# Performance work log

Hardware: AMD Instinct MI355X
Metric: run time of the kernel (lower is better)

The kernel has to match this reference:

```python
import jax, jax.numpy as jnp
import numpy as np

ALPHA = 0.2  # LeakyReLU negative slope
NEG_INF = -9e15

def setup_inputs() -> dict:
    key = jax.random.key(0)
    k1, k2, k3, k4 = jax.random.split(key, 4)
    N, IN_F, OUT_F = 12288, 256, 128
    h = jax.random.normal(k1, (N, IN_F), dtype=jnp.float32)
    adj = jax.random.randint(k2, (N, N), 0, 2, dtype=jnp.int32)
    # Xavier-uniform-like init with gain 1.414
    limW = 1.414 * np.sqrt(6.0 / (IN_F + OUT_F))
    W = jax.random.uniform(k3, (IN_F, OUT_F), dtype=jnp.float32, minval=-limW, maxval=limW)
    lima = 1.414 * np.sqrt(6.0 / (2 * OUT_F + 1))
    a = jax.random.uniform(k4, (2 * OUT_F, 1), dtype=jnp.float32, minval=-lima, maxval=lima)
    return {"h": h, "adj": adj, "W": W, "a": a}

def reference(h, adj, W, a):
    out_f = W.shape[1]
    Wh = h @ W                      # [N, out_f]
    Wh1 = Wh @ a[:out_f, :]         # [N, 1]
    Wh2 = Wh @ a[out_f:, :]         # [N, 1]
    e = Wh1 + Wh2.T                 # [N, N] broadcast-add scores
    e = jnp.where(e > 0, e, ALPHA * e)  # LeakyReLU
    scores = jnp.where(adj > 0, e, NEG_INF)
    attention = jax.nn.softmax(scores, axis=1)  # dropout is identity at inference
    h_prime = attention @ Wh        # [N, out_f]
    return jax.nn.elu(h_prime)      # concat=True -> ELU
```

## Files before the change

### kernel.cpp

```cpp
#include <hip/hip_runtime.h>

#define NN   12288
#define FIN  256
#define FOUT 128
#define ALPHA 0.2f

typedef __attribute__((ext_vector_type(8))) _Float16 half8v;
typedef __attribute__((ext_vector_type(4))) float float4v;
typedef __attribute__((ext_vector_type(4))) int   int4v;


__global__ __launch_bounds__(128) void k_wh(
    const float* __restrict__ h,
    const float* __restrict__ W,
    const float* __restrict__ a,
    _Float16* __restrict__ WhT2,
    float* __restrict__ Wh1, float* __restrict__ Wh2,
    float* __restrict__ mxArr)
{
    __shared__ float sP1[2][16], sP2[2][16];
    const int t = threadIdx.x;
    const int row0 = blockIdx.x * 16;

    float acc[16];
    #pragma unroll
    for (int r = 0; r < 16; ++r) acc[r] = 0.f;

    const float* hb = h + (size_t)row0 * FIN;
    for (int k = 0; k < FIN; k += 4) {
        const float w0 = W[(k + 0) * FOUT + t];
        const float w1 = W[(k + 1) * FOUT + t];
        const float w2 = W[(k + 2) * FOUT + t];
        const float w3 = W[(k + 3) * FOUT + t];
        #pragma unroll
        for (int r = 0; r < 16; ++r) {
            const float4v hv = *(const float4v*)(hb + r * FIN + k);
            float s = acc[r];
            s = fmaf(hv.x, w0, s);
            s = fmaf(hv.y, w1, s);
            s = fmaf(hv.z, w2, s);
            s = fmaf(hv.w, w3, s);
            acc[r] = s;
        }
    }

    half8v pk0, pk1;
    #pragma unroll
    for (int r = 0; r < 8; ++r)  pk0[r] = (_Float16)acc[r];
    #pragma unroll
    for (int r = 0; r < 8; ++r)  pk1[r] = (_Float16)acc[8 + r];
    _Float16* dst = WhT2 + (size_t)(row0 >> 5) * 4096 + t * 32 + (row0 & 16);
    *(half8v*)(dst)     = pk0;
    *(half8v*)(dst + 8) = pk1;

    const float a1t = a[t];
    const float a2t = a[FOUT + t];
    const int lane = t & 63, wv = t >> 6;
    #pragma unroll
    for (int r = 0; r < 16; ++r) {
        float v1 = acc[r] * a1t;
        float v2 = acc[r] * a2t;
        #pragma unroll
        for (int off = 1; off < 64; off <<= 1) {
            v1 += __shfl_xor(v1, off, 64);
            v2 += __shfl_xor(v2, off, 64);
        }
        if (lane == 0) { sP1[wv][r] = v1; sP2[wv][r] = v2; }
    }
    __syncthreads();
    if (t < 16) {
        const float v1 = sP1[0][t] + sP1[1][t];
        float v2 = sP2[0][t] + sP2[1][t];
        Wh1[row0 + t] = v1;
        Wh2[row0 + t] = v2;
        #pragma unroll
        for (int off = 1; off < 16; off <<= 1)
            v2 = fmaxf(v2, __shfl_xor(v2, off, 64));
        if (t == 0) mxArr[blockIdx.x] = v2;
    }
}

static __device__ __forceinline__ half8v build_p(
    const int4v a0, const int4v a1, const float* wvv,
    const float wh1, const float M, float& S)
{
    const int av[8] = {a0.x, a0.y, a0.z, a0.w, a1.x, a1.y, a1.z, a1.w};
    half8v af;
    #pragma unroll
    for (int jj = 0; jj < 8; ++jj) {
        float e = wh1 + wvv[jj];
        e = fmaxf(e, ALPHA * e);
        const float p = av[jj] ? __expf(e - M) : 0.f;
        af[jj] = (_Float16)p;
        S += p;
    }
    return af;
}

static __device__ __forceinline__ float block_gmax(
    const float* __restrict__ mxArr, int nmx, float* smax)
{
    const int tid = threadIdx.x;
    float mv = -1e30f;
    for (int idx = tid; idx < nmx; idx += 256) mv = fmaxf(mv, mxArr[idx]);
    #pragma unroll
    for (int off = 1; off < 64; off <<= 1) mv = fmaxf(mv, __shfl_xor(mv, off, 64));
    if ((tid & 63) == 0) smax[tid >> 6] = mv;
    __syncthreads();
    return fmaxf(fmaxf(smax[0], smax[1]), fmaxf(smax[2], smax[3]));
}

__global__ __launch_bounds__(256, 3) void k_attn(
    const int* __restrict__ adj,
    const _Float16* __restrict__ WhT2,
    const float* __restrict__ Wh1, const float* __restrict__ Wh2,
    const float* __restrict__ mxArr, int nmx,
    float* __restrict__ pC, float* __restrict__ pS)
{
    __shared__ float smax[4];
    const int tid  = threadIdx.x;
    const int w    = tid >> 6;
    const int lane = tid & 63;
    const int m    = lane & 15;
    const int q    = lane >> 4;
    const int rowbase = blockIdx.x * 64 + w * 16;
    const int J    = gridDim.y;
    const int jy   = blockIdx.y;
    const int jlen = NN / J;
    const int jbeg = jy * jlen;

    const float mxv = block_gmax(mxArr, nmx, smax);

    const float wh1 = Wh1[rowbase + m];
    const float tm  = wh1 + mxv;
    const float Mi  = fmaxf(tm, ALPHA * tm);
    const int* rowA = adj + (size_t)(rowbase + m) * NN;

    float4v c[8];
    #pragma unroll
    for (int t = 0; t < 8; ++t) c[t] = (float4v){0.f, 0.f, 0.f, 0.f};
    float S = 0.f;

    for (int j0 = jbeg; j0 < jbeg + jlen; j0 += 32) {
        const int jb = j0 + q * 8;
        const int4v a0 = __builtin_nontemporal_load((const int4v*)(rowA + jb));
        const int4v a1 = __builtin_nontemporal_load((const int4v*)(rowA + jb + 4));
        const float4v w0 = *(const float4v*)(Wh2 + jb);
        const float4v w1 = *(const float4v*)(Wh2 + jb + 4);
        const float wvv[8] = {w0.x, w0.y, w0.z, w0.w, w1.x, w1.y, w1.z, w1.w};

        const half8v af = build_p(a0, a1, wvv, wh1, Mi, S);

        const _Float16* tp = WhT2 + (size_t)(j0 >> 5) * 4096;
        #pragma unroll
        for (int t = 0; t < 8; ++t) {
            const half8v b = *(const half8v*)(tp + (t * 16 + m) * 32 + q * 8);
            c[t] = __builtin_amdgcn_mfma_f32_16x16x32_f16(af, b, c[t], 0, 0, 0);
        }
    }

    S += __shfl_xor(S, 16, 64);
    S += __shfl_xor(S, 32, 64);
    if (q == 0) pS[(size_t)jy * NN + rowbase + m] = S;

    #pragma unroll
    for (int t = 0; t < 8; ++t)
        #pragma unroll
        for (int reg = 0; reg < 4; ++reg) {
            const int row = rowbase + q * 4 + reg;
            pC[((size_t)jy * NN + row) * FOUT + t * 16 + m] = c[t][reg];
        }
}

__global__ __launch_bounds__(256) void k_reduce(
    const float* __restrict__ pC, const float* __restrict__ pS,
    float* __restrict__ out, int J)
{
    const int idx = blockIdx.x * 256 + threadIdx.x;
    const int row = idx >> 5;
    const int c4  = (idx & 31) * 4;
    float4v acc = (float4v){0.f, 0.f, 0.f, 0.f};
    float S = 0.f;
    for (int j = 0; j < J; ++j) {
        const float4v v = *(const float4v*)(pC + ((size_t)j * NN + row) * FOUT + c4);
        acc.x += v.x; acc.y += v.y; acc.z += v.z; acc.w += v.w;
        S += pS[(size_t)j * NN + row];
    }
    const float inv = 1.f / fmaxf(S, 1e-30f);
    float4v r;
    #pragma unroll
    for (int k = 0; k < 4; ++k) {
        const float v = acc[k] * inv;
        r[k] = (v > 0.f) ? v : (__expf(v) - 1.f);
    }
    *(float4v*)(out + (size_t)row * FOUT + c4) = r;
}

__global__ __launch_bounds__(256, 3) void k_attn_fb(
    const int* __restrict__ adj,
    const _Float16* __restrict__ WhT2,
    const float* __restrict__ Wh1, const float* __restrict__ Wh2,
    const float* __restrict__ mxArr, int nmx,
    float* __restrict__ out)
{
    __shared__ float smax[4];
    const int tid  = threadIdx.x;
    const int w    = tid >> 6;
    const int lane = tid & 63;
    const int m    = lane & 15;
    const int q    = lane >> 4;
    const int rowbase = blockIdx.x * 64 + w * 16;

    const float mxv = block_gmax(mxArr, nmx, smax);

    const float wh1 = Wh1[rowbase + m];
    const float tm  = wh1 + mxv;
    const float Mi  = fmaxf(tm, ALPHA * tm);
    const int* rowA = adj + (size_t)(rowbase + m) * NN;

    float4v c[8];
    #pragma unroll
    for (int t = 0; t < 8; ++t) c[t] = (float4v){0.f, 0.f, 0.f, 0.f};
    float S = 0.f;

    for (int j0 = 0; j0 < NN; j0 += 32) {
        const int jb = j0 + q * 8;
        const int4v a0 = __builtin_nontemporal_load((const int4v*)(rowA + jb));
        const int4v a1 = __builtin_nontemporal_load((const int4v*)(rowA + jb + 4));
        const float4v w0 = *(const float4v*)(Wh2 + jb);
        const float4v w1 = *(const float4v*)(Wh2 + jb + 4);
        const float wvv[8] = {w0.x, w0.y, w0.z, w0.w, w1.x, w1.y, w1.z, w1.w};
        const half8v af = build_p(a0, a1, wvv, wh1, Mi, S);
        const _Float16* tp = WhT2 + (size_t)(j0 >> 5) * 4096;
        #pragma unroll
        for (int t = 0; t < 8; ++t) {
            const half8v b = *(const half8v*)(tp + (t * 16 + m) * 32 + q * 8);
            c[t] = __builtin_amdgcn_mfma_f32_16x16x32_f16(af, b, c[t], 0, 0, 0);
        }
    }
    S += __shfl_xor(S, 16, 64);
    S += __shfl_xor(S, 32, 64);
    #pragma unroll
    for (int reg = 0; reg < 4; ++reg) {
        const int mloc = q * 4 + reg;
        const float Sr = __shfl(S, mloc, 64);
        const float inv = 1.f / fmaxf(Sr, 1e-30f);
        #pragma unroll
        for (int t = 0; t < 8; ++t) {
            const float v = c[t][reg] * inv;
            out[(size_t)(rowbase + mloc) * FOUT + t * 16 + m] =
                (v > 0.f) ? v : (__expf(v) - 1.f);
        }
    }
}

extern "C" void kernel_launch(void* const* d_in, const int* in_sizes, int n_in,
                              void* d_out, int out_size, void* d_ws, size_t ws_size,
                              hipStream_t stream) {
    const float* h   = (const float*)d_in[0];
    const int*   adj = (const int*)d_in[1];
    const float* W   = (const float*)d_in[2];
    const float* a   = (const float*)d_in[3];
    float* out = (float*)d_out;

    char* ws = (char*)d_ws;
    float* Wh1   = (float*)ws;
    float* Wh2   = (float*)(ws + 49152);
    float* mxArr = (float*)(ws + 98304);
    _Float16* WhT2 = (_Float16*)(ws + 101376);
    const size_t base_need = 101376ULL + 3145728ULL;
    const int NB = NN / 16;

    int J = 8;
    while (J > 1 &&
           base_need + (size_t)J * NN * 4 + (size_t)J * NN * FOUT * 4 > ws_size)
        J >>= 1;
    const bool ok =
        base_need + (size_t)NN * 4 + (size_t)NN * FOUT * 4 <= ws_size;

    k_wh<<<NB, 128, 0, stream>>>(h, W, a, WhT2, Wh1, Wh2, mxArr);
    if (ok) {
        float* pS = (float*)(ws + base_need);
        float* pC = pS + (size_t)J * NN;
        k_attn<<<dim3(NN / 64, J), 256, 0, stream>>>(adj, WhT2, Wh1, Wh2,
                                                     mxArr, NB, pC, pS);
        k_reduce<<<(NN * (FOUT / 4)) / 256, 256, 0, stream>>>(pC, pS, out, J);
    } else {
        k_attn_fb<<<NN / 64, 256, 0, stream>>>(adj, WhT2, Wh1, Wh2, mxArr, NB, out);
    }
}
```

Baseline: 1.048 ms.

## Process 64 rows per wave to reuse WhT2 B-fragments across four row groups

Each block becomes a single 64-lane wave that handles four 16-row groups. It loads the WhT2 B fragments and Wh2 once per 32-column step and reuses them for all four groups' MFMAs. This cuts redundant global/L2 reads of WhT2, which were repeated by four waves, and replaces the block-level max reduction with a wave-only one with no barrier. In exchange it needs 128 accumulator registers plus the B and adj buffers, so register pressure and occupancy drop, with launch bounds moving from (256,3) to (64,2).

Result: faster. 1.016 ms (-3.1%).

```diff
diff --git a/kernel.cpp b/kernel.cpp
--- a/kernel.cpp
+++ b/kernel.cpp
@@ -97,79 +97,96 @@
     return af;
 }
 
-static __device__ __forceinline__ float block_gmax(
-    const float* __restrict__ mxArr, int nmx, float* smax)
-{
-    const int tid = threadIdx.x;
+static __device__ __forceinline__ float wave_gmax(
+    const float* __restrict__ mxArr, int nmx, int lane)
+{
     float mv = -1e30f;
-    for (int idx = tid; idx < nmx; idx += 256) mv = fmaxf(mv, mxArr[idx]);
-    #pragma unroll
-    for (int off = 1; off < 64; off <<= 1) mv = fmaxf(mv, __shfl_xor(mv, off, 64));
-    if ((tid & 63) == 0) smax[tid >> 6] = mv;
-    __syncthreads();
-    return fmaxf(fmaxf(smax[0], smax[1]), fmaxf(smax[2], smax[3]));
-}
-
-__global__ __launch_bounds__(256, 3) void k_attn(
+    for (int idx = lane; idx < nmx; idx += 64) mv = fmaxf(mv, mxArr[idx]);
+    #pragma unroll
+    for (int off = 1; off < 64; off <<= 1)
+        mv = fmaxf(mv, __shfl_xor(mv, off, 64));
+    return mv;
+}
+
+__global__ __launch_bounds__(64, 2) void k_attn(
     const int* __restrict__ adj,
     const _Float16* __restrict__ WhT2,
     const float* __restrict__ Wh1, const float* __restrict__ Wh2,
     const float* __restrict__ mxArr, int nmx,
     float* __restrict__ pC, float* __restrict__ pS)
 {
-    __shared__ float smax[4];
-    const int tid  = threadIdx.x;
-    const int w    = tid >> 6;
-    const int lane = tid & 63;
+    const int lane = threadIdx.x;
     const int m    = lane & 15;
     const int q    = lane >> 4;
-    const int rowbase = blockIdx.x * 64 + w * 16;
+    const int rowbase = blockIdx.x * 64;
     const int J    = gridDim.y;
     const int jy   = blockIdx.y;
     const int jlen = NN / J;
     const int jbeg = jy * jlen;
 
-    const float mxv = block_gmax(mxArr, nmx, smax);
-
-    const float wh1 = Wh1[rowbase + m];
-    const float tm  = wh1 + mxv;
-    const float Mi  = fmaxf(tm, ALPHA * tm);
-    const int* rowA = adj + (size_t)(rowbase + m) * NN;
-
-    float4v c[8];
-    #pragma unroll
-    for (int t = 0; t < 8; ++t) c[t] = (float4v){0.f, 0.f, 0.f, 0.f};
-    float S = 0.f;
+    const float mxv = wave_gmax(mxArr, nmx, lane);
+
+    float wh1[4], Mi[4];
+    const int* rowp[4];
+    #pragma unroll
+    for (int rg = 0; rg < 4; ++rg) {
+        const int row = rowbase + rg * 16 + m;
+        wh1[rg] = Wh1[row];
+        const float tm = wh1[rg] + mxv;
+        Mi[rg] = fmaxf(tm, ALPHA * tm);
+        rowp[rg] = adj + (size_t)row * NN;
+    }
+
+    float4v c[4][8];
+    #pragma unroll
+    for (int rg = 0; rg < 4; ++rg)
+        #pragma unroll
+        for (int t = 0; t < 8; ++t) c[rg][t] = (float4v){0.f, 0.f, 0.f, 0.f};
+    float S[4] = {0.f, 0.f, 0.f, 0.f};
 
     for (int j0 = jbeg; j0 < jbeg + jlen; j0 += 32) {
         const int jb = j0 + q * 8;
-        const int4v a0 = __builtin_nontemporal_load((const int4v*)(rowA + jb));
-        const int4v a1 = __builtin_nontemporal_load((const int4v*)(rowA + jb + 4));
+
+        int4v a0[4], a1[4];
+        #pragma unroll
+        for (int rg = 0; rg < 4; ++rg) {
+            a0[rg] = __builtin_nontemporal_load((const int4v*)(rowp[rg] + jb));
+            a1[rg] = __builtin_nontemporal_load((const int4v*)(rowp[rg] + jb + 4));
+        }
+        const _Float16* tp = WhT2 + (size_t)(j0 >> 5) * 4096;
+        half8v b[8];
+        #pragma unroll
+        for (int t = 0; t < 8; ++t)
+            b[t] = *(const half8v*)(tp + (t * 16 + m) * 32 + q * 8);
         const float4v w0 = *(const float4v*)(Wh2 + jb);
         const float4v w1 = *(const float4v*)(Wh2 + jb + 4);
         const float wvv[8] = {w0.x, w0.y, w0.z, w0.w, w1.x, w1.y, w1.z, w1.w};
 
-        const half8v af = build_p(a0, a1, wvv, wh1, Mi, S);
-
-        const _Float16* tp = WhT2 + (size_t)(j0 >> 5) * 4096;
-        #pragma unroll
-        for (int t = 0; t < 8; ++t) {
-            const half8v b = *(const half8v*)(tp + (t * 16 + m) * 32 + q * 8);
-            c[t] = __builtin_amdgcn_mfma_f32_16x16x32_f16(af, b, c[t], 0, 0, 0);
-        }
-    }
-
-    S += __shfl_xor(S, 16, 64);
-    S += __shfl_xor(S, 32, 64);
-    if (q == 0) pS[(size_t)jy * NN + rowbase + m] = S;
-
-    #pragma unroll
-    for (int t = 0; t < 8; ++t)
-        #pragma unroll
-        for (int reg = 0; reg < 4; ++reg) {
-            const int row = rowbase + q * 4 + reg;
-            pC[((size_t)jy * NN + row) * FOUT + t * 16 + m] = c[t][reg];
-        }
+        #pragma unroll
+        for (int rg = 0; rg < 4; ++rg) {
+            const half8v af = build_p(a0[rg], a1[rg], wvv, wh1[rg], Mi[rg], S[rg]);
+            #pragma unroll
+            for (int t = 0; t < 8; ++t)
+                c[rg][t] = __builtin_amdgcn_mfma_f32_16x16x32_f16(af, b[t], c[rg][t], 0, 0, 0);
+        }
+    }
+
+    #pragma unroll
+    for (int rg = 0; rg < 4; ++rg) {
+        S[rg] += __shfl_xor(S[rg], 16, 64);
+        S[rg] += __shfl_xor(S[rg], 32, 64);
+        if (q == 0) pS[(size_t)jy * NN + rowbase + rg * 16 + m] = S[rg];
+    }
+
+    #pragma unroll
+    for (int rg = 0; rg < 4; ++rg)
+        #pragma unroll
+        for (int t = 0; t < 8; ++t)
+            #pragma unroll
+            for (int reg = 0; reg < 4; ++reg) {
+                const int row = rowbase + rg * 16 + q * 4 + reg;
+                pC[((size_t)jy * NN + row) * FOUT + t * 16 + m] = c[rg][t][reg];
+            }
 }
 
 __global__ __launch_bounds__(256) void k_reduce(
@@ -196,60 +213,78 @@
     *(float4v*)(out + (size_t)row * FOUT + c4) = r;
 }
 
-__global__ __launch_bounds__(256, 3) void k_attn_fb(
+__global__ __launch_bounds__(64, 2) void k_attn_fb(
     const int* __restrict__ adj,
     const _Float16* __restrict__ WhT2,
     const float* __restrict__ Wh1, const float* __restrict__ Wh2,
     const float* __restrict__ mxArr, int nmx,
     float* __restrict__ out)
 {
-    __shared__ float smax[4];
-    const int tid  = threadIdx.x;
-    const int w    = tid >> 6;
-    const int lane = tid & 63;
+    const int lane = threadIdx.x;
     const int m    = lane & 15;
     const int q    = lane >> 4;
-    const int rowbase = blockIdx.x * 64 + w * 16;
-
-    const float mxv = block_gmax(mxArr, nmx, smax);
-
-    const float wh1 = Wh1[rowbase + m];
-    const float tm  = wh1 + mxv;
-    const float Mi  = fmaxf(tm, ALPHA * tm);
-    const int* rowA = adj + (size_t)(rowbase + m) * NN;
-
-    float4v c[8];
-    #pragma unroll
-    for (int t = 0; t < 8; ++t) c[t] = (float4v){0.f, 0.f, 0.f, 0.f};
-    float S = 0.f;
+    const int rowbase = blockIdx.x * 64;
+
+    const float mxv = wave_gmax(mxArr, nmx, lane);
+
+    float wh1[4], Mi[4];
+    const int* rowp[4];
+    #pragma unroll
+    for (int rg = 0; rg < 4; ++rg) {
+        const int row = rowbase + rg * 16 + m;
+        wh1[rg] = Wh1[row];
+        const float tm = wh1[rg] + mxv;
+        Mi[rg] = fmaxf(tm, ALPHA * tm);
+        rowp[rg] = adj + (size_t)row * NN;
+    }
+
+    float4v c[4][8];
+    #pragma unroll
+    for (int rg = 0; rg < 4; ++rg)
+        #pragma unroll
+        for (int t = 0; t < 8; ++t) c[rg][t] = (float4v){0.f, 0.f, 0.f, 0.f};
+    float S[4] = {0.f, 0.f, 0.f, 0.f};
 
     for (int j0 = 0; j0 < NN; j0 += 32) {
         const int jb = j0 + q * 8;
-        const int4v a0 = __builtin_nontemporal_load((const int4v*)(rowA + jb));
-        const int4v a1 = __builtin_nontemporal_load((const int4v*)(rowA + jb + 4));
+        int4v a0[4], a1[4];
+        #pragma unroll
+        for (int rg = 0; rg < 4; ++rg) {
+            a0[rg] = __builtin_nontemporal_load((const int4v*)(rowp[rg] + jb));
+            a1[rg] = __builtin_nontemporal_load((const int4v*)(rowp[rg] + jb + 4));
+        }
+        const _Float16* tp = WhT2 + (size_t)(j0 >> 5) * 4096;
+        half8v b[8];
+        #pragma unroll
+        for (int t = 0; t < 8; ++t)
+            b[t] = *(const half8v*)(tp + (t * 16 + m) * 32 + q * 8);
         const float4v w0 = *(const float4v*)(Wh2 + jb);
         const float4v w1 = *(const float4v*)(Wh2 + jb + 4);
         const float wvv[8] = {w0.x, w0.y, w0.z, w0.w, w1.x, w1.y, w1.z, w1.w};
-        const half8v af = build_p(a0, a1, wvv, wh1, Mi, S);
-        const _Float16* tp = WhT2 + (size_t)(j0 >> 5) * 4096;
-        #pragma unroll
-        for (int t = 0; t < 8; ++t) {
-            const half8v b = *(const half8v*)(tp + (t * 16 + m) * 32 + q * 8);
-            c[t] = __builtin_amdgcn_mfma_f32_16x16x32_f16(af, b, c[t], 0, 0, 0);
-        }
-    }
-    S += __shfl_xor(S, 16, 64);
-    S += __shfl_xor(S, 32, 64);
-    #pragma unroll
-    for (int reg = 0; reg < 4; ++reg) {
-        const int mloc = q * 4 + reg;
-        const float Sr = __shfl(S, mloc, 64);
-        const float inv = 1.f / fmaxf(Sr, 1e-30f);
-        #pragma unroll
-        for (int t = 0; t < 8; ++t) {
-            const float v = c[t][reg] * inv;
-            out[(size_t)(rowbase + mloc) * FOUT + t * 16 + m] =
-                (v > 0.f) ? v : (__expf(v) - 1.f);
+        #pragma unroll
+        for (int rg = 0; rg < 4; ++rg) {
+            const half8v af = build_p(a0[rg], a1[rg], wvv, wh1[rg], Mi[rg], S[rg]);
+            #pragma unroll
+            for (int t = 0; t < 8; ++t)
+                c[rg][t] = __builtin_amdgcn_mfma_f32_16x16x32_f16(af, b[t], c[rg][t], 0, 0, 0);
+        }
+    }
+
+    #pragma unroll
+    for (int rg = 0; rg < 4; ++rg) {
+        S[rg] += __shfl_xor(S[rg], 16, 64);
+        S[rg] += __shfl_xor(S[rg], 32, 64);
+        #pragma unroll
+        for (int reg = 0; reg < 4; ++reg) {
+            const int mloc = q * 4 + reg;
+            const float Sr = __shfl(S[rg], mloc, 64);
+            const float inv = 1.f / fmaxf(Sr, 1e-30f);
+            #pragma unroll
+            for (int t = 0; t < 8; ++t) {
+                const float v = c[rg][t][reg] * inv;
+                out[(size_t)(rowbase + rg * 16 + mloc) * FOUT + t * 16 + m] =
+                    (v > 0.f) ? v : (__expf(v) - 1.f);
+            }
         }
     }
 }
@@ -282,10 +317,10 @@
     if (ok) {
         float* pS = (float*)(ws + base_need);
         float* pC = pS + (size_t)J * NN;
-        k_attn<<<dim3(NN / 64, J), 256, 0, stream>>>(adj, WhT2, Wh1, Wh2,
-                                                     mxArr, NB, pC, pS);
+        k_attn<<<dim3(NN / 64, J), 64, 0, stream>>>(adj, WhT2, Wh1, Wh2,
+                                                    mxArr, NB, pC, pS);
         k_reduce<<<(NN * (FOUT / 4)) / 256, 256, 0, stream>>>(pC, pS, out, J);
     } else {
-        k_attn_fb<<<NN / 64, 256, 0, stream>>>(adj, WhT2, Wh1, Wh2, mxArr, NB, out);
-    }
-}
+        k_attn_fb<<<NN / 64, 64, 0, stream>>>(adj, WhT2, Wh1, Wh2, mxArr, NB, out);
+    }
+}
```
